# Kernel tuning notes

Measured on AMD Instinct MI355X. Metric: run time of the kernel, lower is better.

The kernel has to match this reference:

```python
import jax, jax.numpy as jnp
import numpy as np

B, S, DIM, H = 2, 2048, 1024, 16
HD = DIM // H  # head dim = 64


def setup_inputs() -> dict:
    key = jax.random.key(0)
    ks = jax.random.split(key, 10)
    scale = 1.0 / np.sqrt(DIM)
    x = jax.random.normal(ks[0], (B, S, DIM), dtype=jnp.float32)
    # per-head projection weights stacked over heads: [H, DIM, HD]
    Wq = jax.random.normal(ks[1], (H, DIM, HD), dtype=jnp.float32) * scale
    bq = jax.random.normal(ks[2], (H, HD), dtype=jnp.float32) * 0.01
    Wk = jax.random.normal(ks[3], (H, DIM, HD), dtype=jnp.float32) * scale
    bk = jax.random.normal(ks[4], (H, HD), dtype=jnp.float32) * 0.01
    Wv = jax.random.normal(ks[5], (H, DIM, HD), dtype=jnp.float32) * scale
    bv = jax.random.normal(ks[6], (H, HD), dtype=jnp.float32) * 0.01
    # output linear: [DIM, DIM]
    Wo = jax.random.normal(ks[7], (DIM, DIM), dtype=jnp.float32) * scale
    bo = jax.random.normal(ks[8], (DIM,), dtype=jnp.float32) * 0.01
    return {"x": x, "Wq": Wq, "bq": bq, "Wk": Wk, "bk": bk,
            "Wv": Wv, "bv": bv, "Wo": Wo, "bo": bo}


def reference(x, Wq, bq, Wk, bk, Wv, bv, Wo, bo):
    # per-head projections: [B, H, S, HD]
    q = jnp.einsum('bsd,hde->bhse', x, Wq) + bq[None, :, None, :]
    k = jnp.einsum('bsd,hde->bhse', x, Wk) + bk[None, :, None, :]
    v = jnp.einsum('bsd,hde->bhse', x, Wv) + bv[None, :, None, :]
    # causal attention scores: [B, H, S, S], scaled by sqrt(head_dim)
    scores = jnp.einsum('bhse,bhte->bhst', q, k) / jnp.sqrt(jnp.float32(HD))
    causal = jnp.tril(jnp.ones((S, S), dtype=bool))
    scores = jnp.where(causal[None, None], scores, -jnp.inf)
    attn = jax.nn.softmax(scores, axis=-1)
    out = jnp.einsum('bhst,bhte->bhse', attn, v)  # [B, H, S, HD]
    # concat heads in order -> [B, S, DIM]
    out = out.transpose(0, 2, 1, 3).reshape(B, S, DIM)
    return out @ Wo + bo
```

## Files before the change

### kernel.cpp

```cpp
#include <hip/hip_runtime.h>

typedef _Float16 half8 __attribute__((ext_vector_type(8)));
typedef _Float16 half4 __attribute__((ext_vector_type(4)));
typedef float f32x4 __attribute__((ext_vector_type(4)));

#define MFMA32(a, b, c) __builtin_amdgcn_mfma_f32_16x16x32_f16((a), (b), (c), 0, 0, 0)
#define MFMA16(a, b, c) __builtin_amdgcn_mfma_f32_16x16x16f16((a), (b), (c), 0, 0, 0)

static constexpr int Bc = 2, Sc = 2048, DIMc = 1024, Hc = 16, HDc = 64;
static constexpr int Mc = Bc * Sc;
static constexpr int NQKV = 3 * DIMc;

__device__ __forceinline__ void gl_lds16(const _Float16* g, _Float16* l) {
  __builtin_amdgcn_global_load_lds(
      (const __attribute__((address_space(1))) void*)g,
      (__attribute__((address_space(3))) void*)l, 16, 0, 0);
}


__global__ __launch_bounds__(256) void k_prep_all(
    const float* __restrict__ x, const float* __restrict__ Wq,
    const float* __restrict__ Wk, const float* __restrict__ Wv,
    const float* __restrict__ Wo, _Float16* __restrict__ xh,
    _Float16* __restrict__ WallT, _Float16* __restrict__ WoT) {
  __shared__ float Ls[64 * 65];
  const int bx = blockIdx.x, tid = threadIdx.x;
  if (bx < 16384) {
    int i = bx * 256 + tid;
    xh[i] = (_Float16)x[i];
    return;
  }
  int b2 = bx - 16384;
  if (b2 < 768) {
    const int dt = b2 & 15, ph = b2 >> 4;
    const int p = ph >> 4, h = ph & 15;
    const float* W = (p == 0) ? Wq : (p == 1) ? Wk : Wv;
    for (int c = tid; c < 4096; c += 256) {
      int dr = c >> 6, e = c & 63;
      Ls[e * 65 + dr] = W[h * 65536 + (dt * 64 + dr) * 64 + e];
    }
    __syncthreads();
    for (int c = tid; c < 4096; c += 256) {
      int e = c >> 6, dr = c & 63;
      WallT[(size_t)(p * 1024 + h * 64 + e) * 1024 + dt * 64 + dr] = (_Float16)Ls[e * 65 + dr];
    }
  } else {
    int b3 = b2 - 768;
    const int dt = b3 & 15, nt = b3 >> 4;
    for (int c = tid; c < 4096; c += 256) {
      int dr = c >> 6, nl = c & 63;
      Ls[nl * 65 + dr] = Wo[(dt * 64 + dr) * 1024 + nt * 64 + nl];
    }
    __syncthreads();
    for (int c = tid; c < 4096; c += 256) {
      int nl = c >> 6, dr = c & 63;
      WoT[(size_t)(nt * 64 + nl) * 1024 + dt * 64 + dr] = (_Float16)Ls[nl * 65 + dr];
    }
  }
}


#define GEMM_CORE()                                                            \
  __shared__ _Float16 As[128 * 64];                                            \
  __shared__ _Float16 Bs[128 * 64];                                            \
  const int tid = threadIdx.x;                                                 \
  const int lane = tid & 63, wave = tid >> 6;                                  \
  const int quad = lane >> 4, mr = lane & 15, m7 = mr & 7;                     \
  const int wm = wave >> 1, wn = wave & 1;                                     \
  f32x4 acc[4][4];                                                             \
  for (int i = 0; i < 4; i++)                                                  \
    for (int j = 0; j < 4; j++) acc[i][j] = f32x4{0.f, 0.f, 0.f, 0.f};         \
  for (int k0 = 0; k0 < DIMc; k0 += 64) {                                      \
    __syncthreads();                                                           \
    for (int it = 0; it < 4; ++it) {                                           \
      int idx = it * 256 + tid;                                                \
      int row = idx >> 3, scb = (idx & 7) ^ (row & 7);                         \
      gl_lds16(&A[(size_t)(m0 + row) * DIMc + k0 + scb * 8],                   \
               &As[(it * 256 + wave * 64) * 8]);                               \
    }                                                                          \
    for (int it = 0; it < 4; ++it) {                                           \
      int idx = it * 256 + tid;                                                \
      int row = idx >> 3, scb = (idx & 7) ^ (row & 7);                         \
      gl_lds16(&Bt[(size_t)(n0 + row) * DIMc + k0 + scb * 8],                  \
               &Bs[(it * 256 + wave * 64) * 8]);                               \
    }                                                                          \
    __syncthreads();                                                           \
    for (int kk = 0; kk < 2; ++kk) {                                           \
      half8 af[4], bf[4];                                                      \
      for (int i = 0; i < 4; i++)                                              \
        af[i] = *(const half8*)&As[(wm * 64 + i * 16 + mr) * 64 +              \
                                   (((kk * 4 + quad) ^ m7) * 8)];              \
      for (int i = 0; i < 4; i++)                                              \
        bf[i] = *(const half8*)&Bs[(wn * 64 + i * 16 + mr) * 64 +              \
                                   (((kk * 4 + quad) ^ m7) * 8)];              \
      for (int i = 0; i < 4; i++)                                              \
        for (int j = 0; j < 4; j++) acc[i][j] = MFMA32(af[i], bf[j], acc[i][j]); \
    }                                                                          \
  }

__global__ __launch_bounds__(256) void k_gemm_qkv(
    const _Float16* __restrict__ xh, const _Float16* __restrict__ WallT,
    const float* __restrict__ bq, const float* __restrict__ bk,
    const float* __restrict__ bv, _Float16* __restrict__ qh,
    _Float16* __restrict__ kh, _Float16* __restrict__ vT) {
  const int id = blockIdx.x;
  const bool qkrole = id < 512;
  const _Float16* A;
  const _Float16* Bt;
  int m0, n0;
  if (qkrole) {
    A = xh; Bt = WallT;
    n0 = (id & 15) * 128; m0 = (id >> 4) * 128;
  } else {
    int j = id - 512;
    A = WallT + (size_t)2048 * DIMc; Bt = xh;
    n0 = (j & 31) * 128; m0 = (j >> 5) * 128;
  }
  GEMM_CORE()
  if (qkrole) {
    for (int i = 0; i < 4; i++) {
      for (int j = 0; j < 4; j++) {
        int col = n0 + wn * 64 + j * 16 + mr;
        int p = col >> 10, rem = col & 1023;
        const float* bias = p ? bk : bq;
        _Float16* dst = p ? kh : qh;
        float bb = bias[rem];
        int h = rem >> 6, e = rem & 63;
        for (int r = 0; r < 4; r++) {
          int row = m0 + wm * 64 + i * 16 + quad * 4 + r;
          int b = row >> 11, s = row & 2047;
          dst[(((size_t)(b * Hc + h)) * Sc + s) * HDc + e] = (_Float16)(acc[i][j][r] + bb);
        }
      }
    }
  } else {
    for (int i = 0; i < 4; i++) {
      int rowb = m0 + wm * 64 + i * 16 + quad * 4;
      for (int j = 0; j < 4; j++) {
        int col = n0 + wn * 64 + j * 16 + mr;
        int b = col >> 11, s = col & 2047;
        for (int r = 0; r < 4; r++) {
          int row = rowb + r;
          vT[(size_t)(b * 1024 + row) * Sc + s] = (_Float16)(acc[i][j][r] + bv[row]);
        }
      }
    }
  }
}

__global__ __launch_bounds__(256) void k_gemm_out(
    const _Float16* __restrict__ A, const _Float16* __restrict__ Bt,
    const float* __restrict__ bo, float* __restrict__ out) {
  const int m0 = blockIdx.y * 128, n0 = blockIdx.x * 128;
  GEMM_CORE()
  for (int i = 0; i < 4; i++) {
    for (int j = 0; j < 4; j++) {
      int col = n0 + wn * 64 + j * 16 + mr;
      float bb = bo[col];
      for (int r = 0; r < 4; r++) {
        int row = m0 + wm * 64 + i * 16 + quad * 4 + r;
        out[(size_t)row * DIMc + col] = acc[i][j][r] + bb;
      }
    }
  }
}


__global__ __launch_bounds__(128, 2) void k_attn(
    const _Float16* __restrict__ qg, const _Float16* __restrict__ kg,
    const _Float16* __restrict__ vTg, _Float16* __restrict__ att) {
  const int xb = blockIdx.x;
  const int qt = (xb & 1) ? (xb >> 1) : (31 - (xb >> 1));
  const int bh = blockIdx.y;
  const int b = bh >> 4, h = bh & 15;
  const int tid = threadIdx.x, wave = tid >> 6, lane = tid & 63;
  const int quad = lane >> 4, mr = lane & 15, m7 = mr & 7;
  const size_t base = (size_t)bh * (Sc * HDc);
  const size_t vbase = ((size_t)b * 1024 + h * 64) * Sc;

  __shared__ _Float16 Ks[2][64 * 64];
  __shared__ _Float16 Vt[2][64 * 64];

  const int q0 = qt * 64 + wave * 32;

  const _Float16 qsc = (_Float16)(0.125f * 1.44269504f);
  half8 aq[2][2];
  for (int qf = 0; qf < 2; ++qf)
    for (int c = 0; c < 2; ++c) {
      half8 v = *(const half8*)&qg[base + (size_t)(q0 + qf * 16 + mr) * 64 + c * 32 + quad * 8];
      for (int j = 0; j < 8; ++j) v[j] = v[j] * qsc;
      aq[qf][c] = v;
    }

  f32x4 o[4][2], ol[2];
  for (int nf = 0; nf < 4; ++nf)
    for (int qf = 0; qf < 2; ++qf) o[nf][qf] = f32x4{0.f, 0.f, 0.f, 0.f};
  ol[0] = ol[1] = f32x4{0.f, 0.f, 0.f, 0.f};
  const half4 ones = {(_Float16)1.f, (_Float16)1.f, (_Float16)1.f, (_Float16)1.f};

  const int nt = qt + 1;

  for (int it = 0; it < 4; ++it) {
    int idx = it * 128 + tid;
    int row = idx >> 3, scb = (idx & 7) ^ (row & 7);
    gl_lds16(kg + base + (size_t)row * 64 + scb * 8, &Ks[0][(it * 128 + wave * 64) * 8]);
  }
  for (int it = 0; it < 4; ++it) {
    int idx = it * 128 + tid;
    int row = idx >> 3, scb = (idx & 7) ^ (row & 7);
    gl_lds16(vTg + vbase + (size_t)row * Sc + scb * 8, &Vt[0][(it * 128 + wave * 64) * 8]);
  }
  __syncthreads();

  for (int t = 0; t < nt; ++t) {
    const int cur = t & 1;
    if (t + 1 < nt) {
      const int nxt = cur ^ 1;
      const _Float16* ks = kg + base + (size_t)(t + 1) * (64 * 64);
      const _Float16* vs = vTg + vbase + (t + 1) * 64;
      for (int it = 0; it < 4; ++it) {
        int idx = it * 128 + tid;
        int row = idx >> 3, scb = (idx & 7) ^ (row & 7);
        gl_lds16(ks + (size_t)row * 64 + scb * 8, &Ks[nxt][(it * 128 + wave * 64) * 8]);
      }
      for (int it = 0; it < 4; ++it) {
        int idx = it * 128 + tid;
        int row = idx >> 3, scb = (idx & 7) ^ (row & 7);
        gl_lds16(vs + (size_t)row * Sc + scb * 8, &Vt[nxt][(it * 128 + wave * 64) * 8]);
      }
    }

    f32x4 sf[2][4];
    for (int kf = 0; kf < 4; ++kf) {
      const int r0 = (kf * 16 + mr) * 64;
      half8 k0 = *(const half8*)&Ks[cur][r0 + ((quad ^ m7) * 8)];
      half8 k1 = *(const half8*)&Ks[cur][r0 + (((quad ^ 4) ^ m7) * 8)];
      for (int qf = 0; qf < 2; ++qf) {
        f32x4 z = {0.f, 0.f, 0.f, 0.f};
        z = MFMA32(k0, aq[qf][0], z);
        z = MFMA32(k1, aq[qf][1], z);
        sf[qf][kf] = z;
      }
    }

    const bool diag = (t == qt);
    half4 pf[2][4];
    for (int qf = 0; qf < 2; ++qf) {
      const int q = q0 + qf * 16 + mr;
      for (int kf = 0; kf < 4; ++kf) {
        half4 pp;
        const int kvb = t * 64 + kf * 16 + quad * 4;
        for (int r = 0; r < 4; ++r) {
          float p = __builtin_amdgcn_exp2f(sf[qf][kf][r]);
          if (diag && (kvb + r > q)) p = 0.f;
          pp[r] = (_Float16)p;
        }
        pf[qf][kf] = pp;
      }
    }

    for (int nf = 0; nf < 4; ++nf) {
      const int er = (nf * 16 + mr) * 64;
      for (int kc = 0; kc < 4; ++kc) {
        int kb = kc * 2 + (quad >> 1);
        half4 vv = *(const half4*)&Vt[cur][er + ((kb ^ m7) * 8) + (quad & 1) * 4];
        for (int qf = 0; qf < 2; ++qf) o[nf][qf] = MFMA16(vv, pf[qf][kc], o[nf][qf]);
      }
    }
    for (int kc = 0; kc < 4; ++kc)
      for (int qf = 0; qf < 2; ++qf) ol[qf] = MFMA16(ones, pf[qf][kc], ol[qf]);

    __syncthreads();
  }

  for (int qf = 0; qf < 2; ++qf) {
    const float inv = 1.0f / ol[qf][0];
    const int q = q0 + qf * 16 + mr;
    for (int nf = 0; nf < 4; ++nf) {
      half4 ov;
      for (int r = 0; r < 4; ++r) ov[r] = (_Float16)(o[nf][qf][r] * inv);
      *(half4*)&att[((size_t)(b * Sc + q)) * DIMc + h * 64 + nf * 16 + quad * 4] = ov;
    }
  }
}


extern "C" void kernel_launch(void* const* d_in, const int* in_sizes, int n_in,
                              void* d_out, int out_size, void* d_ws, size_t ws_size,
                              hipStream_t stream) {
  const float* x  = (const float*)d_in[0];
  const float* Wq = (const float*)d_in[1];
  const float* bq = (const float*)d_in[2];
  const float* Wk = (const float*)d_in[3];
  const float* bk = (const float*)d_in[4];
  const float* Wv = (const float*)d_in[5];
  const float* bv = (const float*)d_in[6];
  const float* Wo = (const float*)d_in[7];
  const float* bo = (const float*)d_in[8];
  float* out = (float*)d_out;

  _Float16* p = (_Float16*)d_ws;
  _Float16* xh    = p; p += (size_t)Mc * DIMc;
  _Float16* WallT = p; p += (size_t)NQKV * DIMc;
  _Float16* WoT   = p; p += (size_t)DIMc * DIMc;
  _Float16* qh    = p; p += (size_t)Bc * Hc * Sc * HDc;
  _Float16* kh    = p; p += (size_t)Bc * Hc * Sc * HDc;
  _Float16* vT    = p; p += (size_t)Bc * Hc * Sc * HDc;
  _Float16* atth  = p;

  k_prep_all<<<16384 + 768 + 256, 256, 0, stream>>>(x, Wq, Wk, Wv, Wo, xh, WallT, WoT);
  k_gemm_qkv<<<768, 256, 0, stream>>>(xh, WallT, bq, bk, bv, qh, kh, vT);
  k_attn<<<dim3(32, Bc * Hc), 128, 0, stream>>>(qh, kh, vT, atth);
  k_gemm_out<<<dim3(DIMc / 128, Mc / 128), 256, 0, stream>>>(atth, WoT, bo, out);
}
```

Measured before the change: 222.3 us.

## Load K/V fragments directly into registers, pair causal query tiles per block

Result: slower. 429.3 us (+93.1%).

```diff
diff --git a/kernel.cpp b/kernel.cpp
--- a/kernel.cpp
+++ b/kernel.cpp
@@ -166,22 +166,20 @@
 }
 
 
-__global__ __launch_bounds__(128, 2) void k_attn(
+__global__ __launch_bounds__(256, 2) void k_attn(
     const _Float16* __restrict__ qg, const _Float16* __restrict__ kg,
     const _Float16* __restrict__ vTg, _Float16* __restrict__ att) {
-  const int xb = blockIdx.x;
-  const int qt = (xb & 1) ? (xb >> 1) : (31 - (xb >> 1));
-  const int bh = blockIdx.y;
+  const int bx = blockIdx.x;
+  const int bh = bx >> 4, qtp = bx & 15;
+  const int wave = threadIdx.x >> 6, lane = threadIdx.x & 63;
+  const int qt = (wave < 2) ? qtp : (31 - qtp);
+  const int strip = wave & 1;
   const int b = bh >> 4, h = bh & 15;
-  const int tid = threadIdx.x, wave = tid >> 6, lane = tid & 63;
-  const int quad = lane >> 4, mr = lane & 15, m7 = mr & 7;
+  const int quad = lane >> 4, mr = lane & 15;
   const size_t base = (size_t)bh * (Sc * HDc);
-  const size_t vbase = ((size_t)b * 1024 + h * 64) * Sc;
-
-  __shared__ _Float16 Ks[2][64 * 64];
-  __shared__ _Float16 Vt[2][64 * 64];
-
-  const int q0 = qt * 64 + wave * 32;
+  const _Float16* __restrict__ vrow = vTg + ((size_t)b * 1024 + h * 64 + mr) * Sc;
+
+  const int q0 = qt * 64 + strip * 32;
 
   const _Float16 qsc = (_Float16)(0.125f * 1.44269504f);
   half8 aq[2][2];
@@ -200,48 +198,36 @@
 
   const int nt = qt + 1;
 
-  for (int it = 0; it < 4; ++it) {
-    int idx = it * 128 + tid;
-    int row = idx >> 3, scb = (idx & 7) ^ (row & 7);
-    gl_lds16(kg + base + (size_t)row * 64 + scb * 8, &Ks[0][(it * 128 + wave * 64) * 8]);
-  }
-  for (int it = 0; it < 4; ++it) {
-    int idx = it * 128 + tid;
-    int row = idx >> 3, scb = (idx & 7) ^ (row & 7);
-    gl_lds16(vTg + vbase + (size_t)row * Sc + scb * 8, &Vt[0][(it * 128 + wave * 64) * 8]);
-  }
-  __syncthreads();
+  half8 kfr[2][4][2];
+  half4 vfr[2][4][4];
+#define LOAD_TILE(buf, t)                                                     \
+  {                                                                           \
+    const _Float16* kp = kg + base + (size_t)(t) * (64 * 64);                 \
+    for (int kf = 0; kf < 4; ++kf)                                            \
+      for (int c = 0; c < 2; ++c)                                             \
+        kfr[buf][kf][c] =                                                     \
+            *(const half8*)&kp[(kf * 16 + mr) * 64 + c * 32 + quad * 8];      \
+    for (int nf = 0; nf < 4; ++nf)                                            \
+      for (int kc = 0; kc < 4; ++kc)                                          \
+        vfr[buf][nf][kc] =                                                    \
+            *(const half4*)&vrow[(size_t)nf * 16 * Sc + (t) * 64 + kc * 16 +  \
+                                 quad * 4];                                   \
+  }
+
+  LOAD_TILE(0, 0)
 
   for (int t = 0; t < nt; ++t) {
     const int cur = t & 1;
-    if (t + 1 < nt) {
-      const int nxt = cur ^ 1;
-      const _Float16* ks = kg + base + (size_t)(t + 1) * (64 * 64);
-      const _Float16* vs = vTg + vbase + (t + 1) * 64;
-      for (int it = 0; it < 4; ++it) {
-        int idx = it * 128 + tid;
-        int row = idx >> 3, scb = (idx & 7) ^ (row & 7);
-        gl_lds16(ks + (size_t)row * 64 + scb * 8, &Ks[nxt][(it * 128 + wave * 64) * 8]);
-      }
-      for (int it = 0; it < 4; ++it) {
-        int idx = it * 128 + tid;
-        int row = idx >> 3, scb = (idx & 7) ^ (row & 7);
-        gl_lds16(vs + (size_t)row * Sc + scb * 8, &Vt[nxt][(it * 128 + wave * 64) * 8]);
-      }
-    }
+    if (t + 1 < nt) LOAD_TILE(cur ^ 1, t + 1)
 
     f32x4 sf[2][4];
-    for (int kf = 0; kf < 4; ++kf) {
-      const int r0 = (kf * 16 + mr) * 64;
-      half8 k0 = *(const half8*)&Ks[cur][r0 + ((quad ^ m7) * 8)];
-      half8 k1 = *(const half8*)&Ks[cur][r0 + (((quad ^ 4) ^ m7) * 8)];
+    for (int kf = 0; kf < 4; ++kf)
       for (int qf = 0; qf < 2; ++qf) {
         f32x4 z = {0.f, 0.f, 0.f, 0.f};
-        z = MFMA32(k0, aq[qf][0], z);
-        z = MFMA32(k1, aq[qf][1], z);
+        z = MFMA32(kfr[cur][kf][0], aq[qf][0], z);
+        z = MFMA32(kfr[cur][kf][1], aq[qf][1], z);
         sf[qf][kf] = z;
       }
-    }
 
     const bool diag = (t == qt);
     half4 pf[2][4];
@@ -259,18 +245,12 @@
       }
     }
 
-    for (int nf = 0; nf < 4; ++nf) {
-      const int er = (nf * 16 + mr) * 64;
-      for (int kc = 0; kc < 4; ++kc) {
-        int kb = kc * 2 + (quad >> 1);
-        half4 vv = *(const half4*)&Vt[cur][er + ((kb ^ m7) * 8) + (quad & 1) * 4];
-        for (int qf = 0; qf < 2; ++qf) o[nf][qf] = MFMA16(vv, pf[qf][kc], o[nf][qf]);
-      }
-    }
+    for (int nf = 0; nf < 4; ++nf)
+      for (int kc = 0; kc < 4; ++kc)
+        for (int qf = 0; qf < 2; ++qf)
+          o[nf][qf] = MFMA16(vfr[cur][nf][kc], pf[qf][kc], o[nf][qf]);
     for (int kc = 0; kc < 4; ++kc)
       for (int qf = 0; qf < 2; ++qf) ol[qf] = MFMA16(ones, pf[qf][kc], ol[qf]);
-
-    __syncthreads();
   }
 
   for (int qf = 0; qf < 2; ++qf) {
@@ -310,6 +290,6 @@
 
   k_prep_all<<<16384 + 768 + 256, 256, 0, stream>>>(x, Wq, Wk, Wv, Wo, xh, WallT, WoT);
   k_gemm_qkv<<<768, 256, 0, stream>>>(xh, WallT, bq, bk, bv, qh, kh, vT);
-  k_attn<<<dim3(32, Bc * Hc), 128, 0, stream>>>(qh, kh, vT, atth);
+  k_attn<<<512, 256, 0, stream>>>(qh, kh, vT, atth);
   k_gemm_out<<<dim3(DIMc / 128, Mc / 128), 256, 0, stream>>>(atth, WoT, bo, out);
 }
```
